# Performance work log

Measured on AMD Instinct MI355X. Metric: run time of the kernel, lower is better.

Reference implementation:

```python
import jax, jax.numpy as jnp
import numpy as np

COLOR_SIZE = 4
SIZE = 64
FILTERS = 512
LENGTH = SIZE * SIZE * 3  # 12288


def setup_inputs() -> dict:
    key = jax.random.key(0)
    k1, k2, k3 = jax.random.split(key, 3)
    example = jax.random.randint(k1, (8, SIZE, SIZE, 3), 0, COLOR_SIZE, dtype=jnp.int32)
    kernel = jax.random.normal(k2, (FILTERS, LENGTH), dtype=jnp.float32)
    bias = jnp.zeros((FILTERS,), dtype=jnp.float32)
    dense_w = jax.random.normal(k3, (FILTERS, COLOR_SIZE), dtype=jnp.float32) * 0.02
    dense_b = jnp.zeros((COLOR_SIZE,), dtype=jnp.float32)
    return {"example": example, "kernel": kernel, "bias": bias,
            "dense_w": dense_w, "dense_b": dense_b}


def reference(example, kernel, bias, dense_w, dense_b):
    B = example.shape[0]
    L = kernel.shape[1]  # 12288
    # normalize int pixels to [-1, 1)
    x = example.astype(jnp.float32) / COLOR_SIZE * 2.0 - 1.0
    x = x.reshape(B, L)                                   # [B, L]
    # FFT-based long (causal full) convolution, fft_length = 2L
    Xf = jnp.fft.rfft(x, n=2 * L, axis=-1)                # [B, L+1] complex64
    Kf = jnp.fft.rfft(kernel, n=2 * L, axis=-1)           # [F, L+1]
    y = jnp.fft.irfft(Xf[:, None, :] * Kf[None, :, :], n=2 * L, axis=-1)[..., :L]  # [B, F, L]
    y = jnp.transpose(y, (0, 2, 1)) + bias                # [B, L, F]
    y = jax.nn.relu(y)
    out = y @ dense_w + dense_b                           # [B, L, color_size]
    return out.reshape(B, SIZE, SIZE, 3, COLOR_SIZE).astype(jnp.float32)
```

## Files before the change

kernel.cpp:

```cpp
#include <hip/hip_runtime.h>

#define FF 512
#define LL 12288
#define NJC 1556
#define NR 128

typedef _Float16 half8 __attribute__((ext_vector_type(8)));
typedef float    f32x4 __attribute__((ext_vector_type(4)));

__global__ __launch_bounds__(256) void prologue(const float* __restrict__ kern,
                                                _Float16* __restrict__ At,
                                                const int* __restrict__ ex,
                                                _Float16* __restrict__ XB,
                                                const float* __restrict__ db,
                                                float* __restrict__ out) {
    int bxx = blockIdx.x;
    if (bxx < 3072) {
        int tid  = bxx * 256 + threadIdx.x;
        int lane = tid & 63;
        int rest = tid >> 6;
        int dc   = rest % 384;
        int ft   = rest / 384;
        int f    = ft * 16 + (lane & 15);
        int d0   = dc * 32 + (lane >> 4) * 8;
        const float* src = kern + (size_t)f * LL + d0;
        half8 v;
#pragma unroll
        for (int i = 0; i < 8; ++i) v[i] = (_Float16)src[i];
        ((half8*)At)[tid] = v;
    } else if (bxx < 3850) {
        int tid = (bxx - 3072) * 256 + threadIdx.x;
        if (tid >= NJC * NR) return;
        int r  = tid & 127;
        int jc = tid >> 7;
        int s  = r >> 3, b = r & 7;
        int j0 = jc * 8;
        half8 v;
#pragma unroll
        for (int i = 0; i < 8; ++i) {
            int idx = LL - 1 - (j0 + i) - s;
            float x = 0.f;
            if (idx >= 0) x = (float)ex[b * LL + idx] * 0.5f - 1.0f;
            v[i] = (_Float16)x;
        }
        ((half8*)XB)[tid] = v;
    } else {
        int tid = (bxx - 3850) * 256 + threadIdx.x;
        out[tid] = db[tid & 3];
    }
}

__device__ __forceinline__ void gl_lds16(const half8* g, half8* l) {
    __builtin_amdgcn_global_load_lds((const __attribute__((address_space(1))) void*)g,
                                     (__attribute__((address_space(3))) void*)l, 16, 0, 0);
}

__global__ __launch_bounds__(256, 2) void conv_main(const _Float16* __restrict__ At,
                                                    const _Float16* __restrict__ XB,
                                                    const float* __restrict__ bias,
                                                    const float* __restrict__ dw,
                                                    float* __restrict__ out) {
    __shared__ half8 Abuf[2][4][8][64];

    int bx    = blockIdx.x;
    int slot  = bx & 7;
    int f_blk = slot >> 1;
    int n_blk = 383 - ((bx >> 3) * 2 + (slot & 1));
    int n0 = n_blk << 5;
    int M  = (n_blk + 4) >> 2;

    int tid  = threadIdx.x;
    int lane = tid & 63;
    int wid  = tid >> 6;
    int quad = lane >> 4;
    int bb   = lane & 7;
    int nh   = (lane >> 3) & 1;

    const half8* Ag  = (const half8*)At;
    const half8* ag0 = Ag + ((size_t)(f_blk * 8 + wid) * 384) * 64 + lane;
    const half8* ag1 = Ag + ((size_t)(f_blk * 8 + wid + 4) * 384) * 64 + lane;

    const half8* Bg = (const half8*)XB;
    int jc0 = 1534 - 4 * n_blk + quad - 2 * nh;
    const half8* pB[4];
#pragma unroll
    for (int t = 0; t < 4; ++t) {
        int tt = wid * 4 + t;
        int r  = (15 - tt) * 8 + bb;
        pB[t] = Bg + (size_t)jc0 * 128 + r;
    }

    f32x4 acc[8][4];
#pragma unroll
    for (int r8 = 0; r8 < 8; ++r8)
#pragma unroll
        for (int t = 0; t < 4; ++t) acc[r8][t] = (f32x4){0.f, 0.f, 0.f, 0.f};

#pragma unroll
    for (int sub = 0; sub < 4; ++sub) {
        gl_lds16(ag0 + (size_t)sub * 64, &Abuf[0][sub][wid][lane]);
        gl_lds16(ag1 + (size_t)sub * 64, &Abuf[0][sub][wid + 4][lane]);
    }
    half8 bcur[4], bnxt[4];
#pragma unroll
    for (int t = 0; t < 4; ++t) bcur[t] = pB[t][0];
    __syncthreads();

    for (int mc = 0; mc < M; ++mc) {
        int buf = mc & 1;
        if (mc + 1 < M) {
            size_t oa = (size_t)(mc + 1) * 256;
#pragma unroll
            for (int sub = 0; sub < 4; ++sub) {
                gl_lds16(ag0 + oa + (size_t)sub * 64, &Abuf[buf ^ 1][sub][wid][lane]);
                gl_lds16(ag1 + oa + (size_t)sub * 64, &Abuf[buf ^ 1][sub][wid + 4][lane]);
            }
        }
#pragma unroll
        for (int sub = 0; sub < 4; ++sub) {
            int dc = mc * 4 + sub;
            size_t ob = (size_t)(dc + 1) * 512;
#pragma unroll
            for (int t = 0; t < 4; ++t) bnxt[t] = pB[t][ob];
            half8 a[8];
#pragma unroll
            for (int r8 = 0; r8 < 8; ++r8) a[r8] = Abuf[buf][sub][r8][lane];
            __builtin_amdgcn_s_barrier();
            __builtin_amdgcn_s_setprio(1);
#pragma unroll
            for (int r8 = 0; r8 < 8; ++r8)
#pragma unroll
                for (int t = 0; t < 4; ++t)
                    acc[r8][t] = __builtin_amdgcn_mfma_f32_16x16x32_f16(a[r8], bcur[t], acc[r8][t], 0, 0, 0);
            __builtin_amdgcn_s_setprio(0);
#pragma unroll
            for (int t = 0; t < 4; ++t) bcur[t] = bnxt[t];
        }
        __syncthreads();
    }

    float p[4][4] = {{0.f}};
#pragma unroll
    for (int r8 = 0; r8 < 8; ++r8) {
#pragma unroll
        for (int reg = 0; reg < 4; ++reg) {
            int f = f_blk * 128 + r8 * 16 + quad * 4 + reg;
            float bs = bias[f];
            float4 w = *(const float4*)(dw + (size_t)f * 4);
#pragma unroll
            for (int t = 0; t < 4; ++t) {
                float y = fmaxf(acc[r8][t][reg] + bs, 0.f);
                p[t][0] += y * w.x; p[t][1] += y * w.y;
                p[t][2] += y * w.z; p[t][3] += y * w.w;
            }
        }
    }
#pragma unroll
    for (int t = 0; t < 4; ++t)
#pragma unroll
        for (int c = 0; c < 4; ++c) {
            float v = p[t][c];
            v += __shfl_xor(v, 16, 64);
            v += __shfl_xor(v, 32, 64);
            p[t][c] = v;
        }
    if (quad == 0) {
#pragma unroll
        for (int t = 0; t < 4; ++t) {
            int n = n0 + (wid * 4 + t) + 16 * nh;
            float* o = out + ((size_t)bb * LL + n) * 4;
#pragma unroll
            for (int c = 0; c < 4; ++c) atomicAdd(o + c, p[t][c]);
        }
    }
}

extern "C" void kernel_launch(void* const* d_in, const int* in_sizes, int n_in,
                              void* d_out, int out_size, void* d_ws, size_t ws_size,
                              hipStream_t stream) {
    const int*   ex   = (const int*)d_in[0];
    const float* kern = (const float*)d_in[1];
    const float* bias = (const float*)d_in[2];
    const float* dw   = (const float*)d_in[3];
    const float* db   = (const float*)d_in[4];
    float* out = (float*)d_out;

    _Float16* At = (_Float16*)d_ws;
    _Float16* XB = (_Float16*)((char*)d_ws + (size_t)FF * LL * 2);

    hipLaunchKernelGGL(prologue, dim3(5386), dim3(256), 0, stream,
                       kern, At, ex, XB, db, out);
    hipLaunchKernelGGL(conv_main, dim3(1536), dim3(256), 0, stream, At, XB, bias, dw, out);
}
```

Measured before the change: 500.7 us.

## Halve filter tile per block and pair long/short causal tiles per block

Each block now covers 64 filters instead of 128 and processes two sequence tiles, a long one (383-pp) and a short one (pp), so total work per block is balanced across the triangular causal workload. Accumulator and LDS footprint are halved, and launch bounds move to 3 blocks per CU for higher occupancy. The cost is that each B fragment is reused across only half as many filters, which doubles B global loads relative to the MFMA work, and there are more atomic adds into the output.

```diff
diff --git a/kernel.cpp b/kernel.cpp
--- a/kernel.cpp
+++ b/kernel.cpp
@@ -55,19 +55,16 @@
                                      (__attribute__((address_space(3))) void*)l, 16, 0, 0);
 }
 
-__global__ __launch_bounds__(256, 2) void conv_main(const _Float16* __restrict__ At,
+__global__ __launch_bounds__(256, 3) void conv_main(const _Float16* __restrict__ At,
                                                     const _Float16* __restrict__ XB,
                                                     const float* __restrict__ bias,
                                                     const float* __restrict__ dw,
                                                     float* __restrict__ out) {
-    __shared__ half8 Abuf[2][4][8][64];
+    __shared__ half8 Abuf[2][4][4][64];
 
     int bx    = blockIdx.x;
-    int slot  = bx & 7;
-    int f_blk = slot >> 1;
-    int n_blk = 383 - ((bx >> 3) * 2 + (slot & 1));
-    int n0 = n_blk << 5;
-    int M  = (n_blk + 4) >> 2;
+    int f_blk = bx & 7;
+    int pp    = bx >> 3;
 
     int tid  = threadIdx.x;
     int lane = tid & 63;
@@ -76,101 +73,102 @@
     int bb   = lane & 7;
     int nh   = (lane >> 3) & 1;
 
-    const half8* Ag  = (const half8*)At;
-    const half8* ag0 = Ag + ((size_t)(f_blk * 8 + wid) * 384) * 64 + lane;
-    const half8* ag1 = Ag + ((size_t)(f_blk * 8 + wid + 4) * 384) * 64 + lane;
+    const half8* Ag = (const half8*)At;
+    const half8* ag = Ag + ((size_t)(f_blk * 4 + wid) * 384) * 64 + lane;
+    const half8* Bg = (const half8*)XB;
 
-    const half8* Bg = (const half8*)XB;
-    int jc0 = 1534 - 4 * n_blk + quad - 2 * nh;
-    const half8* pB[4];
+    for (int tile = 0; tile < 2; ++tile) {
+        int n_blk = tile ? pp : 383 - pp;
+        int n0 = n_blk << 5;
+        int M  = (n_blk + 4) >> 2;
+
+        int jc0 = 1534 - 4 * n_blk + quad - 2 * nh;
+        const half8* pB[4];
 #pragma unroll
-    for (int t = 0; t < 4; ++t) {
-        int tt = wid * 4 + t;
-        int r  = (15 - tt) * 8 + bb;
-        pB[t] = Bg + (size_t)jc0 * 128 + r;
-    }
+        for (int t = 0; t < 4; ++t) {
+            int tt = wid * 4 + t;
+            int r  = (15 - tt) * 8 + bb;
+            pB[t] = Bg + (size_t)jc0 * 128 + r;
+        }
 
-    f32x4 acc[8][4];
+        f32x4 acc[4][4];
 #pragma unroll
-    for (int r8 = 0; r8 < 8; ++r8)
+        for (int rf = 0; rf < 4; ++rf)
 #pragma unroll
-        for (int t = 0; t < 4; ++t) acc[r8][t] = (f32x4){0.f, 0.f, 0.f, 0.f};
+            for (int t = 0; t < 4; ++t) acc[rf][t] = (f32x4){0.f, 0.f, 0.f, 0.f};
 
 #pragma unroll
-    for (int sub = 0; sub < 4; ++sub) {
-        gl_lds16(ag0 + (size_t)sub * 64, &Abuf[0][sub][wid][lane]);
-        gl_lds16(ag1 + (size_t)sub * 64, &Abuf[0][sub][wid + 4][lane]);
-    }
-    half8 bcur[4], bnxt[4];
+        for (int sub = 0; sub < 4; ++sub)
+            gl_lds16(ag + (size_t)sub * 64, &Abuf[0][sub][wid][lane]);
+        half8 bcur[4], bnxt[4];
 #pragma unroll
-    for (int t = 0; t < 4; ++t) bcur[t] = pB[t][0];
-    __syncthreads();
+        for (int t = 0; t < 4; ++t) bcur[t] = pB[t][0];
+        __syncthreads();
 
-    for (int mc = 0; mc < M; ++mc) {
-        int buf = mc & 1;
-        if (mc + 1 < M) {
-            size_t oa = (size_t)(mc + 1) * 256;
+        for (int mc = 0; mc < M; ++mc) {
+            int buf = mc & 1;
+            if (mc + 1 < M) {
+                size_t oa = (size_t)(mc + 1) * 256;
+#pragma unroll
+                for (int sub = 0; sub < 4; ++sub)
+                    gl_lds16(ag + oa + (size_t)sub * 64, &Abuf[buf ^ 1][sub][wid][lane]);
+            }
 #pragma unroll
             for (int sub = 0; sub < 4; ++sub) {
-                gl_lds16(ag0 + oa + (size_t)sub * 64, &Abuf[buf ^ 1][sub][wid][lane]);
-                gl_lds16(ag1 + oa + (size_t)sub * 64, &Abuf[buf ^ 1][sub][wid + 4][lane]);
+                int dc = mc * 4 + sub;
+                size_t ob = (size_t)(dc + 1) * 512;
+#pragma unroll
+                for (int t = 0; t < 4; ++t) bnxt[t] = pB[t][ob];
+                half8 a[4];
+#pragma unroll
+                for (int rf = 0; rf < 4; ++rf) a[rf] = Abuf[buf][sub][rf][lane];
+                __builtin_amdgcn_s_barrier();
+                __builtin_amdgcn_s_setprio(1);
+#pragma unroll
+                for (int rf = 0; rf < 4; ++rf)
+#pragma unroll
+                    for (int t = 0; t < 4; ++t)
+                        acc[rf][t] = __builtin_amdgcn_mfma_f32_16x16x32_f16(a[rf], bcur[t], acc[rf][t], 0, 0, 0);
+                __builtin_amdgcn_s_setprio(0);
+#pragma unroll
+                for (int t = 0; t < 4; ++t) bcur[t] = bnxt[t];
+            }
+            __syncthreads();
+        }
+
+        float p[4][4] = {{0.f}};
+#pragma unroll
+        for (int rf = 0; rf < 4; ++rf) {
+#pragma unroll
+            for (int reg = 0; reg < 4; ++reg) {
+                int f = f_blk * 64 + rf * 16 + quad * 4 + reg;
+                float bs = bias[f];
+                float4 w = *(const float4*)(dw + (size_t)f * 4);
+#pragma unroll
+                for (int t = 0; t < 4; ++t) {
+                    float y = fmaxf(acc[rf][t][reg] + bs, 0.f);
+                    p[t][0] += y * w.x; p[t][1] += y * w.y;
+                    p[t][2] += y * w.z; p[t][3] += y * w.w;
+                }
             }
         }
 #pragma unroll
-        for (int sub = 0; sub < 4; ++sub) {
-            int dc = mc * 4 + sub;
-            size_t ob = (size_t)(dc + 1) * 512;
+        for (int t = 0; t < 4; ++t)
 #pragma unroll
-            for (int t = 0; t < 4; ++t) bnxt[t] = pB[t][ob];
-            half8 a[8];
-#pragma unroll
-            for (int r8 = 0; r8 < 8; ++r8) a[r8] = Abuf[buf][sub][r8][lane];
-            __builtin_amdgcn_s_barrier();
-            __builtin_amdgcn_s_setprio(1);
-#pragma unroll
-            for (int r8 = 0; r8 < 8; ++r8)
-#pragma unroll
-                for (int t = 0; t < 4; ++t)
-                    acc[r8][t] = __builtin_amdgcn_mfma_f32_16x16x32_f16(a[r8], bcur[t], acc[r8][t], 0, 0, 0);
-            __builtin_amdgcn_s_setprio(0);
-#pragma unroll
-            for (int t = 0; t < 4; ++t) bcur[t] = bnxt[t];
-        }
-        __syncthreads();
-    }
-
-    float p[4][4] = {{0.f}};
-#pragma unroll
-    for (int r8 = 0; r8 < 8; ++r8) {
-#pragma unroll
-        for (int reg = 0; reg < 4; ++reg) {
-            int f = f_blk * 128 + r8 * 16 + quad * 4 + reg;
-            float bs = bias[f];
-            float4 w = *(const float4*)(dw + (size_t)f * 4);
+            for (int c = 0; c < 4; ++c) {
+                float v = p[t][c];
+                v += __shfl_xor(v, 16, 64);
+                v += __shfl_xor(v, 32, 64);
+                p[t][c] = v;
+            }
+        if (quad == 0) {
 #pragma unroll
             for (int t = 0; t < 4; ++t) {
-                float y = fmaxf(acc[r8][t][reg] + bs, 0.f);
-                p[t][0] += y * w.x; p[t][1] += y * w.y;
-                p[t][2] += y * w.z; p[t][3] += y * w.w;
+                int n = n0 + (wid * 4 + t) + 16 * nh;
+                float* o = out + ((size_t)bb * LL + n) * 4;
+#pragma unroll
+                for (int c = 0; c < 4; ++c) atomicAdd(o + c, p[t][c]);
             }
-        }
-    }
-#pragma unroll
-    for (int t = 0; t < 4; ++t)
-#pragma unroll
-        for (int c = 0; c < 4; ++c) {
-            float v = p[t][c];
-            v += __shfl_xor(v, 16, 64);
-            v += __shfl_xor(v, 32, 64);
-            p[t][c] = v;
-        }
-    if (quad == 0) {
-#pragma unroll
-        for (int t = 0; t < 4; ++t) {
-            int n = n0 + (wid * 4 + t) + 16 * nh;
-            float* o = out + ((size_t)bb * LL + n) * 4;
-#pragma unroll
-            for (int c = 0; c < 4; ++c) atomicAdd(o + c, p[t][c]);
         }
     }
 }
```

Result: slower. 629.6 us (+25.8%).
